# Optimization experiments

Measured on AMD Instinct MI355X. Metric: run time of the kernel, lower is better.

The kernel has to match this reference:

```python
import jax, jax.numpy as jnp
import numpy as np

NUM_NEIGH = 6  # 5 + 1 hardcoded in PeerNet

def pr_transform(h, num_neigh=NUM_NEIGH):
    # h: [B, F]. For each feature column, replace each value by the mean of its
    # num_neigh nearest batch values (by absolute difference, self included).
    def per_feat(col):  # col: [B]
        dist = jnp.abs(col[:, None] - col[None, :])  # [B, B]
        _, idx = jax.lax.top_k(-dist, num_neigh)      # [B, k] nearest indices
        return jnp.mean(col[idx], axis=1)             # [B]
    # lax.map over features keeps peak memory at one [B,B] matrix at a time
    return jax.lax.map(per_feat, h.T).T


def setup_inputs() -> dict:
    key = jax.random.key(0)
    ks = jax.random.split(key, 9)
    B, D = 4096, 1024
    H1, H2, O = 128, 64, 2
    s = 0.02
    return {
        "x":   jax.random.normal(ks[0], (B, D), dtype=jnp.float32),
        "W1":  jax.random.normal(ks[1], (H1, D), dtype=jnp.float32) * s,
        "b1":  jnp.zeros((H1,), dtype=jnp.float32),
        "Wpr": jax.random.normal(ks[2], (H1, H1), dtype=jnp.float32) * s,
        "bpr": jnp.zeros((H1,), dtype=jnp.float32),
        "W2":  jax.random.normal(ks[3], (H2, H1), dtype=jnp.float32) * s,
        "b2":  jnp.zeros((H2,), dtype=jnp.float32),
        "Wo":  jax.random.normal(ks[4], (O, H2), dtype=jnp.float32) * s,
        "bo":  jnp.zeros((O,), dtype=jnp.float32),
    }


def reference(x, W1, b1, Wpr, bpr, W2, b2, Wo, bo):
    # hidden1 + relu (dropout = identity, eval mode)
    h1 = jax.nn.relu(x @ W1.T + b1)               # [B, 128]
    # PRLayer: per-feature kNN averaging over batch, then linear
    pr = pr_transform(h1)                          # [B, 128]
    pr = jax.nn.relu(pr @ Wpr.T + bpr)             # [B, 128]
    h2 = jax.nn.relu(pr @ W2.T + b2)               # [B, 64]
    out = h2 @ Wo.T + bo                           # [B, 2]
    return out
```

## Files before the change

### kernel.cpp

```cpp
#include <hip/hip_runtime.h>


#define NB   4096
#define DIN  1024
#define NH1  128
#define NH2  64

typedef _Float16 f16x8 __attribute__((ext_vector_type(8)));
typedef _Float16 f16x4 __attribute__((ext_vector_type(4)));
typedef float    f32x4 __attribute__((ext_vector_type(4)));

__global__ __launch_bounds__(256) void prep_w1(const float* __restrict__ W1,
                                               _Float16* __restrict__ Whi,
                                               _Float16* __restrict__ Wlo)
{
    const int i = (blockIdx.x * 256 + threadIdx.x) * 4;
    const float4 v = *(const float4*)&W1[i];
    const _Float16 h0 = (_Float16)v.x, h1 = (_Float16)v.y;
    const _Float16 h2 = (_Float16)v.z, h3 = (_Float16)v.w;
    f16x4 hv = {h0, h1, h2, h3};
    f16x4 lv = {(_Float16)(v.x - (float)h0), (_Float16)(v.y - (float)h1),
                (_Float16)(v.z - (float)h2), (_Float16)(v.w - (float)h3)};
    *(f16x4*)&Whi[i] = hv;
    *(f16x4*)&Wlo[i] = lv;
}

__global__ __launch_bounds__(512) void gemm1_mfma(const float* __restrict__ x,
                                                  const _Float16* __restrict__ Whi,
                                                  const _Float16* __restrict__ Wlo,
                                                  const float* __restrict__ b1,
                                                  float* __restrict__ h1T)
{
    __shared__ _Float16 xhi[16 * 1032];
    __shared__ _Float16 xlo[16 * 1032];
    const int tid = threadIdx.x;
    const int m0  = blockIdx.x * 16;

    {
        const int r  = tid >> 5;
        const int kb = (tid & 31) * 4;
#pragma unroll
        for (int i = 0; i < 8; ++i) {
            const int k = kb + i * 128;
            const float4 v = *(const float4*)&x[(size_t)(m0 + r) * DIN + k];
            const _Float16 h0 = (_Float16)v.x, h1 = (_Float16)v.y;
            const _Float16 h2 = (_Float16)v.z, h3 = (_Float16)v.w;
            f16x4 hv = {h0, h1, h2, h3};
            f16x4 lv = {(_Float16)(v.x - (float)h0), (_Float16)(v.y - (float)h1),
                        (_Float16)(v.z - (float)h2), (_Float16)(v.w - (float)h3)};
            *(f16x4*)&xhi[r * 1032 + k] = hv;
            *(f16x4*)&xlo[r * 1032 + k] = lv;
        }
    }
    __syncthreads();

    const int lane = tid & 63;
    const int w    = tid >> 6;
    const int n0   = w * 16;
    const int fr   = lane & 15;
    const int fq   = lane >> 4;

    f32x4 acc = {0.f, 0.f, 0.f, 0.f};
    const _Float16* __restrict__ whp = &Whi[(size_t)(n0 + fr) * DIN + fq * 8];
    const _Float16* __restrict__ wlp = &Wlo[(size_t)(n0 + fr) * DIN + fq * 8];
    const _Float16* xh = &xhi[fr * 1032 + fq * 8];
    const _Float16* xl = &xlo[fr * 1032 + fq * 8];

#pragma unroll 4
    for (int ks = 0; ks < 32; ++ks) {
        const int k = ks * 32;
        const f16x8 ah = *(const f16x8*)&xh[k];
        const f16x8 al = *(const f16x8*)&xl[k];
        const f16x8 bh = *(const f16x8*)&whp[k];
        const f16x8 bl = *(const f16x8*)&wlp[k];
        acc = __builtin_amdgcn_mfma_f32_16x16x32_f16(ah, bh, acc, 0, 0, 0);
        acc = __builtin_amdgcn_mfma_f32_16x16x32_f16(ah, bl, acc, 0, 0, 0);
        acc = __builtin_amdgcn_mfma_f32_16x16x32_f16(al, bh, acc, 0, 0, 0);
    }

    const int n = n0 + fr;
    const float bv = b1[n];
    float4 o;
    o.x = fmaxf(acc[0] + bv, 0.f);
    o.y = fmaxf(acc[1] + bv, 0.f);
    o.z = fmaxf(acc[2] + bv, 0.f);
    o.w = fmaxf(acc[3] + bv, 0.f);
    *(float4*)&h1T[(size_t)n * NB + m0 + fq * 4] = o;
}

__global__ __launch_bounds__(512) void sort_window_kernel(const float* __restrict__ h1T,
                                                          float* __restrict__ prtT)
{
    __shared__ float s[NB];
    const int t    = threadIdx.x;
    const int col  = blockIdx.x >> 1;
    const int half = blockIdx.x & 1;
    const float* __restrict__ src = h1T + (size_t)col * NB;

    float v[8];
    {
        const float4 a = *(const float4*)&src[8 * t];
        const float4 b = *(const float4*)&src[8 * t + 4];
        v[0] = a.x; v[1] = a.y; v[2] = a.z; v[3] = a.w;
        v[4] = b.x; v[5] = b.y; v[6] = b.z; v[7] = b.w;
    }

#define CE(a, b, up)                                        \
    {                                                       \
        const float _x = v[a], _y = v[b];                   \
        v[a] = (up) ? fminf(_x, _y) : fmaxf(_x, _y);        \
        v[b] = (up) ? fmaxf(_x, _y) : fminf(_x, _y);        \
    }

    CE(0, 1, true); CE(2, 3, false); CE(4, 5, true); CE(6, 7, false);
    CE(0, 2, true);  CE(1, 3, true);  CE(4, 6, false); CE(5, 7, false);
    CE(0, 1, true);  CE(2, 3, true);  CE(4, 5, false); CE(6, 7, false);

#pragma unroll
    for (int k = 8; k <= 256; k <<= 1) {
        const bool up = (t & (k >> 3)) == 0;
#pragma unroll
        for (int j = k >> 1; j >= 8; j >>= 1) {
            const int  m       = j >> 3;
            const bool keepmin = (((t & m) == 0) == up);
#pragma unroll
            for (int q = 0; q < 8; ++q) {
                const float p = __shfl_xor(v[q], m);
                v[q] = keepmin ? fminf(v[q], p) : fmaxf(v[q], p);
            }
        }
        CE(0, 4, up); CE(1, 5, up); CE(2, 6, up); CE(3, 7, up);
        CE(0, 2, up); CE(1, 3, up); CE(4, 6, up); CE(5, 7, up);
        CE(0, 1, up); CE(2, 3, up); CE(4, 5, up); CE(6, 7, up);
    }

#pragma unroll
    for (int k = 512; k <= 4096; k <<= 1) {
        const bool up = (t & (k >> 3)) == 0;
#pragma unroll
        for (int j = k >> 1; j >= 512; j >>= 1) {
            __syncthreads();
            float4 w0 = {v[0], v[1], v[2], v[3]};
            float4 w1 = {v[4], v[5], v[6], v[7]};
            *(float4*)&s[8 * t]     = w0;
            *(float4*)&s[8 * t + 4] = w1;
            __syncthreads();
            const int tp = t ^ (j >> 3);
            const float4 pa = *(const float4*)&s[8 * tp];
            const float4 pb = *(const float4*)&s[8 * tp + 4];
            const bool keepmin = (((t & (j >> 3)) == 0) == up);
            const float p[8] = {pa.x, pa.y, pa.z, pa.w, pb.x, pb.y, pb.z, pb.w};
#pragma unroll
            for (int q = 0; q < 8; ++q)
                v[q] = keepmin ? fminf(v[q], p[q]) : fmaxf(v[q], p[q]);
        }
#pragma unroll
        for (int j = 256; j >= 8; j >>= 1) {
            const int  m       = j >> 3;
            const bool keepmin = (((t & m) == 0) == up);
#pragma unroll
            for (int q = 0; q < 8; ++q) {
                const float p = __shfl_xor(v[q], m);
                v[q] = keepmin ? fminf(v[q], p) : fmaxf(v[q], p);
            }
        }
        CE(0, 4, up); CE(1, 5, up); CE(2, 6, up); CE(3, 7, up);
        CE(0, 2, up); CE(1, 3, up); CE(4, 6, up); CE(5, 7, up);
        CE(0, 1, up); CE(2, 3, up); CE(4, 5, up); CE(6, 7, up);
    }
#undef CE

    __syncthreads();
    {
        float4 w0 = {v[0], v[1], v[2], v[3]};
        float4 w1 = {v[4], v[5], v[6], v[7]};
        *(float4*)&s[8 * t]     = w0;
        *(float4*)&s[8 * t + 4] = w1;
    }
    __syncthreads();

    const float z5 = s[5];
#pragma unroll
    for (int p = 0; p < 4; ++p) {
        const int e    = half * 2048 + t + p * 512;
        const float v0 = src[e];
        if (v0 == 0.0f && z5 == 0.0f) {
            prtT[(size_t)col * NB + e] = 0.0f;
            continue;
        }
        int lo = 0, hi = NB;
        while (lo < hi) {
            const int mid = (lo + hi) >> 1;
            if (s[mid] < v0) lo = mid + 1; else hi = mid;
        }
        int l = lo, h = lo;
        float sum = v0;
#pragma unroll
        for (int it = 0; it < 5; ++it) {
            const int li = (l > 0) ? l - 1 : 0;
            const int ri = (h < NB - 1) ? h + 1 : NB - 1;
            const float sl = s[li];
            const float sr = s[ri];
            const float dl = (l > 0) ? (v0 - sl) : 1e30f;
            const float dr = (h < NB - 1) ? (sr - v0) : 1e30f;
            if (dl <= dr) { sum += sl; l = li; }
            else          { sum += sr; h = ri; }
        }
        prtT[(size_t)col * NB + e] = sum * (1.0f / 6.0f);
    }
}

__global__ __launch_bounds__(512) void tail_kernel(const float* __restrict__ AT,
                                                   const float* __restrict__ Wpr,
                                                   const float* __restrict__ bpr,
                                                   const float* __restrict__ W2,
                                                   const float* __restrict__ b2,
                                                   const float* __restrict__ Wo,
                                                   const float* __restrict__ bo,
                                                   float* __restrict__ out)
{
    __shared__ float As[NH1 * 17];
    __shared__ float Bs[NH1 * 132];
    __shared__ float Ps[16 * 132];
    __shared__ float Rs[32 * 32];
    const int tid = threadIdx.x;
    const int m0  = blockIdx.x * 16;

    {
        const int row = tid >> 2;
        const int f   = (tid & 3) * 4;
        const float4 v = *(const float4*)&AT[(size_t)row * NB + m0 + f];
        As[row * 17 + f + 0] = v.x;
        As[row * 17 + f + 1] = v.y;
        As[row * 17 + f + 2] = v.z;
        As[row * 17 + f + 3] = v.w;
    }
    {
        const int n  = tid >> 2;
        const int kb = (tid & 3) * 32;
#pragma unroll
        for (int i4 = 0; i4 < 8; ++i4) {
            const float4 v = *(const float4*)&Wpr[(size_t)n * NH1 + kb + i4 * 4];
            Bs[(kb + i4 * 4 + 0) * 132 + n] = v.x;
            Bs[(kb + i4 * 4 + 1) * 132 + n] = v.y;
            Bs[(kb + i4 * 4 + 2) * 132 + n] = v.z;
            Bs[(kb + i4 * 4 + 3) * 132 + n] = v.w;
        }
    }
    __syncthreads();

    const int m  = tid & 15;
    const int g  = tid >> 4;
    const int n0 = g * 4;

    float acc[4] = {0.f, 0.f, 0.f, 0.f};
#pragma unroll 8
    for (int kk = 0; kk < NH1; ++kk) {
        const float a  = As[kk * 17 + m];
        const float4 b = *(const float4*)&Bs[kk * 132 + n0];
        acc[0] = fmaf(a, b.x, acc[0]);
        acc[1] = fmaf(a, b.y, acc[1]);
        acc[2] = fmaf(a, b.z, acc[2]);
        acc[3] = fmaf(a, b.w, acc[3]);
    }
#pragma unroll
    for (int j = 0; j < 4; ++j)
        Ps[m * 132 + n0 + j] = fmaxf(acc[j] + bpr[n0 + j], 0.f);
    __syncthreads();

    {
        const int j2 = tid >> 3;
        const int nb = (tid & 7) * 16;
#pragma unroll
        for (int i4 = 0; i4 < 4; ++i4) {
            const float4 v = *(const float4*)&W2[(size_t)j2 * NH1 + nb + i4 * 4];
            Bs[(nb + i4 * 4 + 0) * 68 + j2] = v.x;
            Bs[(nb + i4 * 4 + 1) * 68 + j2] = v.y;
            Bs[(nb + i4 * 4 + 2) * 68 + j2] = v.z;
            Bs[(nb + i4 * 4 + 3) * 68 + j2] = v.w;
        }
    }
    __syncthreads();

    const int j0 = g * 2;
    float acc2[2] = {0.f, 0.f};
#pragma unroll 8
    for (int nn = 0; nn < NH1; ++nn) {
        const float p  = Ps[m * 132 + nn];
        const float2 w = *(const float2*)&Bs[nn * 68 + j0];
        acc2[0] = fmaf(p, w.x, acc2[0]);
        acc2[1] = fmaf(p, w.y, acc2[1]);
    }

    float po0 = 0.f, po1 = 0.f;
#pragma unroll
    for (int j = 0; j < 2; ++j) {
        const float h = fmaxf(acc2[j] + b2[j0 + j], 0.f);
        po0 = fmaf(h, Wo[j0 + j], po0);
        po1 = fmaf(h, Wo[NH2 + j0 + j], po1);
    }
    Rs[g * 32 + m * 2 + 0] = po0;
    Rs[g * 32 + m * 2 + 1] = po1;
    __syncthreads();
    if (tid < 32) {
        const int mm = tid >> 1, o = tid & 1;
        float sum = 0.f;
#pragma unroll
        for (int gg = 0; gg < 32; ++gg) sum += Rs[gg * 32 + mm * 2 + o];
        out[(size_t)(m0 + mm) * 2 + o] = sum + bo[o];
    }
}

extern "C" void kernel_launch(void* const* d_in, const int* in_sizes, int n_in,
                              void* d_out, int out_size, void* d_ws, size_t ws_size,
                              hipStream_t stream)
{
    const float* x   = (const float*)d_in[0];
    const float* W1  = (const float*)d_in[1];
    const float* b1  = (const float*)d_in[2];
    const float* Wpr = (const float*)d_in[3];
    const float* bpr = (const float*)d_in[4];
    const float* W2  = (const float*)d_in[5];
    const float* b2  = (const float*)d_in[6];
    const float* Wo  = (const float*)d_in[7];
    const float* bo  = (const float*)d_in[8];

    float* ws     = (float*)d_ws;
    float* h1T    = ws;
    float* prtT   = h1T + NH1 * NB;
    _Float16* Whi = (_Float16*)(prtT + NH1 * NB);
    _Float16* Wlo = Whi + NH1 * DIN;

    prep_w1<<<dim3(NH1 * DIN / 4 / 256), 256, 0, stream>>>(W1, Whi, Wlo);
    gemm1_mfma<<<dim3(NB / 16), 512, 0, stream>>>(x, Whi, Wlo, b1, h1T);
    sort_window_kernel<<<dim3(NH1 * 2), 512, 0, stream>>>(h1T, prtT);
    tail_kernel<<<dim3(NB / 16), 512, 0, stream>>>(prtT, Wpr, bpr, W2, b2, Wo, bo,
                                                   (float*)d_out);
}
```

Measured before the change: 58.36 us.

## Precompute kNN window means in sorted order, then gather via interleaved binary search

After the bitonic sort, each thread computes the 6-nearest-neighbour mean for its 8 sorted positions and stores the results in a second shared array. Each output element then only needs a fixed-depth binary search to find its sorted rank, with four searches interleaved per thread for ILP, followed by one lookup. This removes the divergent per-element window walk after each search. It costs an extra 16KB of shared memory, an extra barrier, and each block now computes window means for the whole column rather than just its half.

```diff
diff --git a/kernel.cpp b/kernel.cpp
--- a/kernel.cpp
+++ b/kernel.cpp
@@ -92,6 +92,7 @@
                                                           float* __restrict__ prtT)
 {
     __shared__ float s[NB];
+    __shared__ float r_[NB];
     const int t    = threadIdx.x;
     const int col  = blockIdx.x >> 1;
     const int half = blockIdx.x & 1;
@@ -179,34 +180,66 @@
     }
     __syncthreads();
 
+    if (v[7] == 0.0f) {
+        const float4 z4 = {0.f, 0.f, 0.f, 0.f};
+        *(float4*)&r_[8 * t]     = z4;
+        *(float4*)&r_[8 * t + 4] = z4;
+    } else {
+        float rr[8];
+#pragma unroll
+        for (int q = 0; q < 8; ++q) {
+            const int  p  = 8 * t + q;
+            const float v0 = v[q];
+            int l = p, h = p;
+            float sum = v0;
+#pragma unroll
+            for (int it = 0; it < 5; ++it) {
+                const int li = (l > 0) ? l - 1 : 0;
+                const int ri = (h < NB - 1) ? h + 1 : NB - 1;
+                const float sl = s[li];
+                const float sr = s[ri];
+                const float dl = (l > 0) ? (v0 - sl) : 1e30f;
+                const float dr = (h < NB - 1) ? (sr - v0) : 1e30f;
+                if (dl <= dr) { sum += sl; l = li; }
+                else          { sum += sr; h = ri; }
+            }
+            rr[q] = sum * (1.0f / 6.0f);
+        }
+        const float4 r0 = {rr[0], rr[1], rr[2], rr[3]};
+        const float4 r1 = {rr[4], rr[5], rr[6], rr[7]};
+        *(float4*)&r_[8 * t]     = r0;
+        *(float4*)&r_[8 * t + 4] = r1;
+    }
+    __syncthreads();
+
     const float z5 = s[5];
-#pragma unroll
-    for (int p = 0; p < 4; ++p) {
-        const int e    = half * 2048 + t + p * 512;
-        const float v0 = src[e];
-        if (v0 == 0.0f && z5 == 0.0f) {
-            prtT[(size_t)col * NB + e] = 0.0f;
-            continue;
-        }
-        int lo = 0, hi = NB;
-        while (lo < hi) {
-            const int mid = (lo + hi) >> 1;
-            if (s[mid] < v0) lo = mid + 1; else hi = mid;
-        }
-        int l = lo, h = lo;
-        float sum = v0;
-#pragma unroll
-        for (int it = 0; it < 5; ++it) {
-            const int li = (l > 0) ? l - 1 : 0;
-            const int ri = (h < NB - 1) ? h + 1 : NB - 1;
-            const float sl = s[li];
-            const float sr = s[ri];
-            const float dl = (l > 0) ? (v0 - sl) : 1e30f;
-            const float dr = (h < NB - 1) ? (sr - v0) : 1e30f;
-            if (dl <= dr) { sum += sl; l = li; }
-            else          { sum += sr; h = ri; }
-        }
-        prtT[(size_t)col * NB + e] = sum * (1.0f / 6.0f);
+    float v0[4];
+    bool  zs[4];
+    float key[4];
+    int   lo[4], hi[4];
+#pragma unroll
+    for (int w = 0; w < 4; ++w) {
+        const int e = half * 2048 + t + w * 512;
+        v0[w]  = src[e];
+        zs[w]  = (v0[w] == 0.0f) && (z5 == 0.0f);
+        key[w] = zs[w] ? -1.0f : v0[w];
+        lo[w]  = 0;
+        hi[w]  = NB;
+    }
+#pragma unroll
+    for (int step = 0; step < 12; ++step) {
+#pragma unroll
+        for (int w = 0; w < 4; ++w) {
+            const int mid = (lo[w] + hi[w]) >> 1;
+            const float sv = s[mid];
+            if (sv < key[w]) lo[w] = mid + 1; else hi[w] = mid;
+        }
+    }
+#pragma unroll
+    for (int w = 0; w < 4; ++w) {
+        const int e = half * 2048 + t + w * 512;
+        const float res = zs[w] ? 0.0f : r_[lo[w]];
+        prtT[(size_t)col * NB + e] = res;
     }
 }
 
```

After: 58.20 us. No clear change (-0.3%).
